# Kernel tuning notes

Measured on AMD Instinct MI355X. Metric: run time of the kernel, lower is better.

The kernel has to match this reference:

```python
import jax, jax.numpy as jnp
import numpy as np

N_NODES = 40000
N_EDGES = 320000
N_GRAPHS = 64
IN_DIM = 128
HID4 = 256   # hidden_dim * 4
OUT_DIM = 128
LN_EPS = 1e-5


def setup_inputs() -> dict:
    key = jax.random.key(0)
    ks = jax.random.split(key, 12)
    x = jax.random.normal(ks[0], (N_NODES, IN_DIM), dtype=jnp.float32)
    w = jax.random.uniform(ks[1], (N_EDGES, 4), dtype=jnp.float32)
    src = jax.random.randint(ks[2], (N_EDGES,), 0, N_NODES, dtype=jnp.int32)
    dst = jax.random.randint(ks[3], (N_EDGES,), 0, N_NODES, dtype=jnp.int32)
    graph_ids = jnp.sort(jax.random.randint(ks[4], (N_NODES,), 0, N_GRAPHS, dtype=jnp.int32))
    # parameters (no biases on GraphConv / fc1 linear)
    W1 = jax.random.normal(ks[5], (IN_DIM, HID4), dtype=jnp.float32) / np.sqrt(IN_DIM)
    fc1_W = jax.random.normal(ks[6], (IN_DIM, HID4), dtype=jnp.float32) / np.sqrt(IN_DIM)
    ln_gamma = jnp.ones((HID4,), dtype=jnp.float32)
    ln_beta = jnp.zeros((HID4,), dtype=jnp.float32)
    W2 = jax.random.normal(ks[7], (2 * HID4, HID4), dtype=jnp.float32) / np.sqrt(2 * HID4)
    W3 = jax.random.normal(ks[8], (HID4, OUT_DIM), dtype=jnp.float32) / np.sqrt(HID4)
    return {"x": x, "w": w, "W1": W1, "fc1_W": fc1_W, "ln_gamma": ln_gamma,
            "ln_beta": ln_beta, "W2": W2, "W3": W3,
            "src": src, "dst": dst, "graph_ids": graph_ids}


def _graph_conv(feat, src, dst, ew, W, out_inv_sqrt, in_inv_sqrt):
    # DGL GraphConv, norm='both', bias=False, with scalar edge_weight:
    # h = D_out^{-1/2} x ; m_e = w_e * h[src] ; agg = scatter_add(m, dst) ;
    # out = (D_in^{-1/2} agg) @ W
    h = feat * out_inv_sqrt[:, None]
    m = h[src] * ew[:, None]                       # [E, D] messages
    agg = jax.ops.segment_sum(m, dst, num_segments=N_NODES)
    return (agg * in_inv_sqrt[:, None]) @ W


def reference(x, w, W1, fc1_W, ln_gamma, ln_beta, W2, W3, src, dst, graph_ids):
    # unweighted degree normalization (DGL uses structural degrees, clamp(min=1))
    ones_e = jnp.ones((N_EDGES,), dtype=x.dtype)
    out_deg = jnp.maximum(jax.ops.segment_sum(ones_e, src, num_segments=N_NODES), 1.0)
    in_deg = jnp.maximum(jax.ops.segment_sum(ones_e, dst, num_segments=N_NODES), 1.0)
    out_inv = out_deg ** -0.5
    in_inv = in_deg ** -0.5

    ew = jnp.max(w, axis=1)                        # [E]

    x1 = jax.nn.relu(_graph_conv(x, src, dst, ew, W1, out_inv, in_inv))

    # fc1: Linear(no bias) -> LayerNorm(affine) -> ReLU
    f1 = x @ fc1_W
    mu = jnp.mean(f1, axis=-1, keepdims=True)
    var = jnp.mean((f1 - mu) ** 2, axis=-1, keepdims=True)
    f1 = (f1 - mu) * jax.lax.rsqrt(var + LN_EPS) * ln_gamma + ln_beta
    f1 = jax.nn.relu(f1)

    x1f1 = jnp.concatenate([x1, f1], axis=1)       # [N, 512]
    x2 = jax.nn.relu(_graph_conv(x1f1, src, dst, ew, W2, out_inv, in_inv))
    x3 = jax.nn.relu(_graph_conv(x2, src, dst, ew, W3, out_inv, in_inv))

    # dgl.sum_nodes over batched graph, then row-wise L2 normalize
    readout = jax.ops.segment_sum(x3, graph_ids, num_segments=N_GRAPHS)  # [G, OUT_DIM]
    norm = jnp.maximum(jnp.linalg.norm(readout, axis=1, keepdims=True), 1e-12)
    return readout / norm
```

## Files before the change

### kernel.cpp

```cpp
#include <hip/hip_runtime.h>

#define N_NODES 40000
#define M_PAD   40064
#define N_EDGES 320000
#define N_GRAPHS 64
#define IN_DIM 128
#define HID4 256
#define OUT_DIM 128
#define LN_EPS 1e-5f

typedef short  s16x8  __attribute__((ext_vector_type(8)));
typedef __bf16 bf16x8 __attribute__((ext_vector_type(8)));
typedef float  f32x4  __attribute__((ext_vector_type(4)));

__device__ __forceinline__ unsigned short f2b(float f) {
    unsigned int u = __builtin_bit_cast(unsigned int, f);
    u += 0x7fffu + ((u >> 16) & 1u);
    return (unsigned short)(u >> 16);
}
__device__ __forceinline__ float b2f(unsigned short h) {
    unsigned int u = (unsigned int)h << 16;
    return __builtin_bit_cast(float, u);
}
__device__ __forceinline__ float lo2f(unsigned int u) { return b2f((unsigned short)u); }
__device__ __forceinline__ float hi2f(unsigned int u) { return b2f((unsigned short)(u >> 16)); }
__device__ __forceinline__ unsigned int packb(float x, float y) {
    return (unsigned int)f2b(x) | ((unsigned int)f2b(y) << 16);
}

__device__ __forceinline__ void gll16(const unsigned short* g, short* lds_base) {
    __builtin_amdgcn_global_load_lds(
        (const __attribute__((address_space(1))) unsigned int*)g,
        (__attribute__((address_space(3))) unsigned int*)lds_base, 16, 0, 0);
}

#define MFMA_BF16(a, b, c) __builtin_amdgcn_mfma_f32_16x16x32_bf16( \
    __builtin_bit_cast(bf16x8, a), __builtin_bit_cast(bf16x8, b), c, 0, 0, 0)


#define XN (N_NODES * IN_DIM)
#define XT (XN / 8)
#define WN 229376
#define PREP_TOT (XT + WN + N_EDGES)

__global__ void prep_all(const float* __restrict__ x, const float* __restrict__ W1,
                         const float* __restrict__ fc1, const float* __restrict__ W2,
                         const float* __restrict__ W3, const float* __restrict__ w,
                         const int* __restrict__ src, const int* __restrict__ dst,
                         unsigned short* __restrict__ xb, unsigned short* __restrict__ W1t,
                         unsigned short* __restrict__ fc1t, unsigned short* __restrict__ W2t,
                         unsigned short* __restrict__ W3t, float* __restrict__ ew,
                         int* __restrict__ cnt_out, int* __restrict__ cnt_in,
                         int* __restrict__ rank) {
    int idx = blockIdx.x * 256 + threadIdx.x;
    if (idx < XT) {
        const float4* xv = (const float4*)x;
        float4 u = xv[idx * 2], v = xv[idx * 2 + 1];
        uint4 o;
        o.x = packb(u.x, u.y); o.y = packb(u.z, u.w);
        o.z = packb(v.x, v.y); o.w = packb(v.z, v.w);
        ((uint4*)xb)[idx] = o;
        return;
    }
    int j = idx - XT;
    if (j < 32768) { int k = j >> 8, n = j & 255; W1t[n * 128 + k] = f2b(W1[j]); return; }
    j -= 32768;
    if (j < 32768) { int k = j >> 8, n = j & 255; fc1t[n * 128 + k] = f2b(fc1[j]); return; }
    j -= 32768;
    if (j < 131072) { int k = j >> 8, n = j & 255; W2t[n * 512 + k] = f2b(W2[j]); return; }
    j -= 131072;
    if (j < 32768) { int k = j >> 7, n = j & 127; W3t[n * 256 + k] = f2b(W3[j]); return; }
    j -= 32768;
    if (j < N_EDGES) {
        float4 v = ((const float4*)w)[j];
        ew[j] = fmaxf(fmaxf(v.x, v.y), fmaxf(v.z, v.w));
        atomicAdd(&cnt_out[src[j]], 1);
        rank[j] = atomicAdd(&cnt_in[dst[j]], 1);
    }
}

__global__ void scan_part(const int* __restrict__ cnt, int* __restrict__ partial) {
    int b = blockIdx.x;
    int s = 0;
    for (int i = threadIdx.x; i < 1000; i += 256) s += cnt[b * 1000 + i];
#pragma unroll
    for (int m = 1; m < 64; m <<= 1) s += __shfl_xor(s, m);
    __shared__ int wsm[4];
    if ((threadIdx.x & 63) == 0) wsm[threadIdx.x >> 6] = s;
    __syncthreads();
    if (threadIdx.x == 0) partial[b] = wsm[0] + wsm[1] + wsm[2] + wsm[3];
}

__global__ void scan_final(const int* __restrict__ cnt_in, const int* __restrict__ cnt_out,
                           const int* __restrict__ partial, int* __restrict__ off,
                           float* __restrict__ out_inv, float* __restrict__ in_inv) {
    int b = blockIdx.x, tid = threadIdx.x;
    int lane = tid & 63, wv = tid >> 6;
    int pre = 0;
    for (int j = 0; j < b; ++j) pre += partial[j];
    int i = b * 1000 + tid;
    int v = (tid < 1000) ? cnt_in[i] : 0;
    int x = v;
#pragma unroll
    for (int ofs = 1; ofs < 64; ofs <<= 1) {
        int t = __shfl_up(x, ofs);
        if (lane >= ofs) x += t;
    }
    __shared__ int wsum[16];
    if (lane == 63) wsum[wv] = x;
    __syncthreads();
    if (wv == 0 && lane < 16) {
        int s = wsum[lane];
#pragma unroll
        for (int ofs = 1; ofs < 16; ofs <<= 1) {
            int t = __shfl_up(s, ofs);
            if (lane >= ofs) s += t;
        }
        wsum[lane] = s;
    }
    __syncthreads();
    int incl = pre + (wv > 0 ? wsum[wv - 1] : 0) + x;
    if (tid < 1000) {
        off[i] = incl - v;
        in_inv[i] = rsqrtf(fmaxf((float)v, 1.0f));
        out_inv[i] = rsqrtf(fmaxf((float)cnt_out[i], 1.0f));
    }
    if (b == 39 && tid == 999) off[N_NODES] = incl;
}

__global__ void csr_fill(const int* __restrict__ src, const int* __restrict__ dst,
                         const float* __restrict__ ew, const float* __restrict__ out_inv,
                         const int* __restrict__ off, const int* __restrict__ rank,
                         int4* __restrict__ es) {
    int e = blockIdx.x * 256 + threadIdx.x;
    if (e >= N_EDGES) return;
    int d = dst[e];
    int slot = off[d] + rank[e];
    int s = src[e];
    float wv = ew[e];
    es[slot] = make_int4(s, __float_as_int(wv * out_inv[s]), __float_as_int(wv), 0);
}


template <int D, int RELU, int WSEL>
__global__ void gather_nodes(const unsigned short* __restrict__ h, const int* __restrict__ off,
                             const int4* __restrict__ eg, const float* __restrict__ scale,
                             unsigned short* __restrict__ outb) {
    int n = blockIdx.x;
    int lane = threadIdx.x;
    int b = off[n], e = off[n + 1];
    const uint2* hu = (const uint2*)h;
    float a0 = 0.f, a1 = 0.f, a2 = 0.f, a3 = 0.f;
    if constexpr (D == 256) {
        int i = b;
        for (; i + 3 < e; i += 4) {
            int4 e0 = eg[i], e1 = eg[i + 1], e2 = eg[i + 2], e3 = eg[i + 3];
            uint2 p0 = hu[(size_t)e0.x * 64 + lane];
            uint2 p1 = hu[(size_t)e1.x * 64 + lane];
            uint2 p2 = hu[(size_t)e2.x * 64 + lane];
            uint2 p3 = hu[(size_t)e3.x * 64 + lane];
            float w0 = __int_as_float(WSEL ? e0.z : e0.y);
            float w1 = __int_as_float(WSEL ? e1.z : e1.y);
            float w2 = __int_as_float(WSEL ? e2.z : e2.y);
            float w3 = __int_as_float(WSEL ? e3.z : e3.y);
            a0 += w0 * lo2f(p0.x) + w1 * lo2f(p1.x) + w2 * lo2f(p2.x) + w3 * lo2f(p3.x);
            a1 += w0 * hi2f(p0.x) + w1 * hi2f(p1.x) + w2 * hi2f(p2.x) + w3 * hi2f(p3.x);
            a2 += w0 * lo2f(p0.y) + w1 * lo2f(p1.y) + w2 * lo2f(p2.y) + w3 * lo2f(p3.y);
            a3 += w0 * hi2f(p0.y) + w1 * hi2f(p1.y) + w2 * hi2f(p2.y) + w3 * hi2f(p3.y);
        }
        for (; i < e; ++i) {
            int4 ee = eg[i];
            uint2 p = hu[(size_t)ee.x * 64 + lane];
            float w0 = __int_as_float(WSEL ? ee.z : ee.y);
            a0 += w0 * lo2f(p.x); a1 += w0 * hi2f(p.x);
            a2 += w0 * lo2f(p.y); a3 += w0 * hi2f(p.y);
        }
        float sc = scale[n];
        a0 *= sc; a1 *= sc; a2 *= sc; a3 *= sc;
        if (RELU) {
            a0 = fmaxf(a0, 0.f); a1 = fmaxf(a1, 0.f);
            a2 = fmaxf(a2, 0.f); a3 = fmaxf(a3, 0.f);
        }
        uint2 o; o.x = packb(a0, a1); o.y = packb(a2, a3);
        ((uint2*)outb)[(size_t)n * 64 + lane] = o;
    } else {
        int half = lane >> 5, cl = lane & 31;
        int i = b;
        for (; i + 3 < e; i += 4) {
            int4 ea = eg[i + half];
            int4 eb = eg[i + 2 + half];
            uint2 pa = hu[(size_t)ea.x * 32 + cl];
            uint2 pb = hu[(size_t)eb.x * 32 + cl];
            float wa = __int_as_float(WSEL ? ea.z : ea.y);
            float wb = __int_as_float(WSEL ? eb.z : eb.y);
            a0 += wa * lo2f(pa.x) + wb * lo2f(pb.x);
            a1 += wa * hi2f(pa.x) + wb * hi2f(pb.x);
            a2 += wa * lo2f(pa.y) + wb * lo2f(pb.y);
            a3 += wa * hi2f(pa.y) + wb * hi2f(pb.y);
        }
        for (; i < e; i += 2) {
            int idx = i + half;
            int4 ee = eg[idx < e ? idx : i];
            float w = (idx < e) ? __int_as_float(WSEL ? ee.z : ee.y) : 0.0f;
            uint2 p = hu[(size_t)ee.x * 32 + cl];
            a0 += w * lo2f(p.x); a1 += w * hi2f(p.x);
            a2 += w * lo2f(p.y); a3 += w * hi2f(p.y);
        }
        a0 += __shfl_xor(a0, 32); a1 += __shfl_xor(a1, 32);
        a2 += __shfl_xor(a2, 32); a3 += __shfl_xor(a3, 32);
        float sc = scale[n];
        a0 *= sc; a1 *= sc; a2 *= sc; a3 *= sc;
        if (RELU) {
            a0 = fmaxf(a0, 0.f); a1 = fmaxf(a1, 0.f);
            a2 = fmaxf(a2, 0.f); a3 = fmaxf(a3, 0.f);
        }
        if (half == 0) {
            uint2 o; o.x = packb(a0, a1); o.y = packb(a2, a3);
            ((uint2*)outb)[(size_t)n * 32 + cl] = o;
        }
    }
}


#define G3_NPB 8

__global__ void gather3_ro(const unsigned short* __restrict__ h, const int* __restrict__ off,
                           const int4* __restrict__ eg, const float* __restrict__ scale,
                           const int* __restrict__ gid, float* __restrict__ ro) {
    int lane = threadIdx.x;
    int half = lane >> 5, cl = lane & 31;
    int n0 = blockIdx.x * G3_NPB;
    int n1 = n0 + G3_NPB;
    if (n1 > N_NODES) n1 = N_NODES;
    const uint2* hu = (const uint2*)h;
    float r0 = 0.f, r1 = 0.f, r2 = 0.f, r3 = 0.f;
    int cur = gid[n0];
    for (int n = n0; n < n1; ++n) {
        int g = gid[n];
        if (g != cur) {
            atomicAdd(&ro[cur * OUT_DIM + 4 * cl + 2 * half], half ? r2 : r0);
            atomicAdd(&ro[cur * OUT_DIM + 4 * cl + 2 * half + 1], half ? r3 : r1);
            r0 = r1 = r2 = r3 = 0.f;
            cur = g;
        }
        int b = off[n], e = off[n + 1];
        float a0 = 0.f, a1 = 0.f, a2 = 0.f, a3 = 0.f;
        int i = b;
        for (; i + 3 < e; i += 4) {
            int4 ea = eg[i + half];
            int4 eb = eg[i + 2 + half];
            uint2 pa = hu[(size_t)ea.x * 32 + cl];
            uint2 pb = hu[(size_t)eb.x * 32 + cl];
            float wa = __int_as_float(ea.z), wb = __int_as_float(eb.z);
            a0 += wa * lo2f(pa.x) + wb * lo2f(pb.x);
            a1 += wa * hi2f(pa.x) + wb * hi2f(pb.x);
            a2 += wa * lo2f(pa.y) + wb * lo2f(pb.y);
            a3 += wa * hi2f(pa.y) + wb * hi2f(pb.y);
        }
        for (; i < e; i += 2) {
            int idx = i + half;
            int4 ee = eg[idx < e ? idx : i];
            float w = (idx < e) ? __int_as_float(ee.z) : 0.0f;
            uint2 p = hu[(size_t)ee.x * 32 + cl];
            a0 += w * lo2f(p.x); a1 += w * hi2f(p.x);
            a2 += w * lo2f(p.y); a3 += w * hi2f(p.y);
        }
        a0 += __shfl_xor(a0, 32); a1 += __shfl_xor(a1, 32);
        a2 += __shfl_xor(a2, 32); a3 += __shfl_xor(a3, 32);
        float sc = scale[n];
        r0 += fmaxf(a0 * sc, 0.0f); r1 += fmaxf(a1 * sc, 0.0f);
        r2 += fmaxf(a2 * sc, 0.0f); r3 += fmaxf(a3 * sc, 0.0f);
    }
    atomicAdd(&ro[cur * OUT_DIM + 4 * cl + 2 * half], half ? r2 : r0);
    atomicAdd(&ro[cur * OUT_DIM + 4 * cl + 2 * half + 1], half ? r3 : r1);
}


__device__ __forceinline__ void gemm_core(short* As, short* Bs,
    const unsigned short* __restrict__ A, const unsigned short* __restrict__ A2,
    const unsigned short* __restrict__ Bt, unsigned short* __restrict__ C,
    const float* __restrict__ rowScaleC, int K1, int K2, int N,
    int relu, int scaleC, int m0, int n0) {
    int tid = threadIdx.x;
    int lane = tid & 63, wave = tid >> 6;
    int wm = (wave >> 1) * 64, wn = (wave & 1) * 64;
    int quad = lane >> 4, r16 = lane & 15;
    const int K = K1 + K2;
    f32x4 acc[4][4] = {};
    int srow = lane >> 3;
    int sk   = ((lane & 7) ^ srow) * 8;
    int xorc = r16 & 7;
    short* ldsA = As + wave * 2048;
    short* ldsB = Bs + wave * 2048;

    for (int k0 = 0; k0 < K; k0 += 64) {
        int kk = k0 + sk;
#pragma unroll
        for (int h = 0; h < 4; ++h) {
            int r = wave * 32 + h * 8 + srow;
            const unsigned short* Ap = (k0 < K1)
                ? A  + (size_t)(m0 + r) * K1 + kk
                : A2 + (size_t)(m0 + r) * K2 + (kk - K1);
            gll16(Ap, ldsA + h * 512);
            gll16(Bt + (size_t)(n0 + r) * K + kk, ldsB + h * 512);
        }
        __syncthreads();
#pragma unroll
        for (int c = 0; c < 2; ++c) {
            s16x8 af[4], bfr[4];
            int pc = (((c * 4 + quad) ^ xorc) << 3);
#pragma unroll
            for (int i = 0; i < 4; ++i)
                af[i] = *(const s16x8*)(As + (wm + i * 16 + r16) * 64 + pc);
#pragma unroll
            for (int j = 0; j < 4; ++j)
                bfr[j] = *(const s16x8*)(Bs + (wn + j * 16 + r16) * 64 + pc);
#pragma unroll
            for (int i = 0; i < 4; ++i)
#pragma unroll
                for (int j = 0; j < 4; ++j)
                    acc[i][j] = MFMA_BF16(af[i], bfr[j], acc[i][j]);
        }
        __syncthreads();
    }

#pragma unroll
    for (int i = 0; i < 4; ++i) {
        int mbase = m0 + wm + i * 16 + quad * 4;
#pragma unroll
        for (int r = 0; r < 4; ++r) {
            int m = mbase + r;
            float sc = scaleC ? rowScaleC[m] : 1.0f;
#pragma unroll
            for (int j = 0; j < 4; ++j) {
                float v = acc[i][j][r] * sc;
                if (relu) v = fmaxf(v, 0.0f);
                C[(size_t)m * N + n0 + wn + j * 16 + r16] = f2b(v);
            }
        }
    }
}

template <int RELU, int SCALE_C>
__global__ __launch_bounds__(256) void gemm_mfma(
    const unsigned short* __restrict__ A, const unsigned short* __restrict__ A2,
    const unsigned short* __restrict__ Bt, unsigned short* __restrict__ C,
    const float* __restrict__ rowScaleC, int K1, int K2, int N) {
    __shared__ short As[8192];
    __shared__ short Bs[8192];
    gemm_core(As, Bs, A, A2, Bt, C, rowScaleC, K1, K2, N, RELU, SCALE_C,
              blockIdx.x * 128, blockIdx.y * 128);
}


__global__ __launch_bounds__(512) void gemm_dual(
    const unsigned short* __restrict__ A0, const unsigned short* __restrict__ B0,
    unsigned short* __restrict__ C0,
    const unsigned short* __restrict__ A1, const unsigned short* __restrict__ B1,
    unsigned short* __restrict__ C1,
    const float* __restrict__ gamma, const float* __restrict__ beta) {
    __shared__ short As[4096];
    __shared__ short Bs[8192];
    __shared__ float lns[128][4];
    __shared__ float lnq[128][4];
    const unsigned short* A  = blockIdx.z ? A1 : A0;
    const unsigned short* Bt = blockIdx.z ? B1 : B0;
    unsigned short* C        = blockIdx.z ? C1 : C0;
    int tid = threadIdx.x;
    int lane = tid & 63, wave = tid >> 6;
    int wm = (wave >> 2) * 64, wn = (wave & 3) * 64;
    int quad = lane >> 4, r16 = lane & 15;
    int m0 = blockIdx.x * 128;
    f32x4 acc[4][4] = {};
    int lrow = lane >> 2;
    int kc = (lane & 3) * 8;
    short* ldsA = As + wave * 512;
    short* ldsB = Bs + wave * 512;

    for (int k0 = 0; k0 < 128; k0 += 32) {
        int kk = k0 + kc;
        int rr = wave * 16 + lrow;
        gll16(A + (size_t)(m0 + rr) * 128 + kk, ldsA);
        gll16(Bt + (size_t)rr * 128 + kk, ldsB);
        gll16(Bt + (size_t)(128 + rr) * 128 + kk, ldsB + 4096);
        __syncthreads();
        s16x8 af[4], bfr[4];
#pragma unroll
        for (int i = 0; i < 4; ++i)
            af[i] = *(const s16x8*)(As + (wm + i * 16 + r16) * 32 + quad * 8);
#pragma unroll
        for (int j = 0; j < 4; ++j)
            bfr[j] = *(const s16x8*)(Bs + (wn + j * 16 + r16) * 32 + quad * 8);
#pragma unroll
        for (int i = 0; i < 4; ++i)
#pragma unroll
            for (int j = 0; j < 4; ++j)
                acc[i][j] = MFMA_BF16(af[i], bfr[j], acc[i][j]);
        __syncthreads();
    }

    if (blockIdx.z == 0) {
#pragma unroll
        for (int i = 0; i < 4; ++i) {
            int mbase = m0 + wm + i * 16 + quad * 4;
#pragma unroll
            for (int r = 0; r < 4; ++r) {
                int m = mbase + r;
#pragma unroll
                for (int j = 0; j < 4; ++j)
                    C[(size_t)m * 256 + wn + j * 16 + r16] = f2b(fmaxf(acc[i][j][r], 0.0f));
            }
        }
    } else {
#pragma unroll
        for (int i = 0; i < 4; ++i)
#pragma unroll
            for (int r = 0; r < 4; ++r) {
                float s = 0.0f, q = 0.0f;
#pragma unroll
                for (int j = 0; j < 4; ++j) { float v = acc[i][j][r]; s += v; q += v * v; }
#pragma unroll
                for (int m = 1; m < 16; m <<= 1) { s += __shfl_xor(s, m); q += __shfl_xor(q, m); }
                if (r16 == 0) {
                    int row = wm + i * 16 + quad * 4 + r;
                    lns[row][wave & 3] = s;
                    lnq[row][wave & 3] = q;
                }
            }
        __syncthreads();
#pragma unroll
        for (int i = 0; i < 4; ++i) {
#pragma unroll
            for (int r = 0; r < 4; ++r) {
                int row = wm + i * 16 + quad * 4 + r;
                float s = lns[row][0] + lns[row][1] + lns[row][2] + lns[row][3];
                float q = lnq[row][0] + lnq[row][1] + lnq[row][2] + lnq[row][3];
                float mu = s * (1.0f / HID4);
                float var = q * (1.0f / HID4) - mu * mu;
                float rs = rsqrtf(var + LN_EPS);
                int m = m0 + row;
#pragma unroll
                for (int j = 0; j < 4; ++j) {
                    int col = wn + j * 16 + r16;
                    float v = (acc[i][j][r] - mu) * rs * gamma[col] + beta[col];
                    C[(size_t)m * 256 + col] = f2b(fmaxf(v, 0.0f));
                }
            }
        }
    }
}


__global__ void normalize_out(const float* __restrict__ ro, float* __restrict__ out) {
    int g = blockIdx.x;
    int d = threadIdx.x;
    float v = ro[g * OUT_DIM + d];
    float ss = v * v;
#pragma unroll
    for (int m = 1; m < 64; m <<= 1) ss += __shfl_xor(ss, m);
    __shared__ float s2[2];
    if ((d & 63) == 0) s2[d >> 6] = ss;
    __syncthreads();
    float tot = s2[0] + s2[1];
    float norm = fmaxf(sqrtf(tot), 1e-12f);
    out[g * OUT_DIM + d] = v / norm;
}


extern "C" void kernel_launch(void* const* d_in, const int* in_sizes, int n_in,
                              void* d_out, int out_size, void* d_ws, size_t ws_size,
                              hipStream_t stream) {
    const float* x    = (const float*)d_in[0];
    const float* w    = (const float*)d_in[1];
    const float* W1   = (const float*)d_in[2];
    const float* fc1W = (const float*)d_in[3];
    const float* gam  = (const float*)d_in[4];
    const float* bet  = (const float*)d_in[5];
    const float* W2   = (const float*)d_in[6];
    const float* W3   = (const float*)d_in[7];
    const int* src = (const int*)d_in[8];
    const int* dst = (const int*)d_in[9];
    const int* gid = (const int*)d_in[10];
    float* out = (float*)d_out;

    float* ws = (float*)d_ws;
    float* out_inv = ws + 0;
    float* in_inv  = ws + 40000;
    float* ew      = ws + 80000;
    int*   cnt_out = (int*)(ws + 400000);
    int*   cnt_in  = (int*)(ws + 440000);
    float* ro      = ws + 480000;
    unsigned short* W1t  = (unsigned short*)(ws + 488192);
    unsigned short* fc1t = (unsigned short*)(ws + 504576);
    unsigned short* W2t  = (unsigned short*)(ws + 520960);
    unsigned short* W3t  = (unsigned short*)(ws + 586496);
    int*   partial = (int*)(ws + 602880);
    int*   off     = (int*)(ws + 602920);
    int4*  es      = (int4*)(ws + 642924);
    unsigned short* xb    = (unsigned short*)(ws + 1923000);
    unsigned short* Q3b   = xb;
    unsigned short* agg1b = (unsigned short*)(ws + 4487100);
    unsigned short* x2b   = agg1b;
    unsigned short* x1b   = (unsigned short*)(ws + 9615300);
    unsigned short* f1b   = (unsigned short*)(ws + 14743500);
    unsigned short* P2b   = (unsigned short*)(ws + 19871700);
    int*   rank    = (int*)(ws + 25000000);

    hipMemsetAsync(cnt_out, 0, (2 * 40000 + N_GRAPHS * OUT_DIM) * sizeof(float), stream);

    prep_all<<<(PREP_TOT + 255) / 256, 256, 0, stream>>>(x, W1, fc1W, W2, W3, w, src, dst,
                                                         xb, W1t, fc1t, W2t, W3t, ew,
                                                         cnt_out, cnt_in, rank);
    scan_part<<<40, 256, 0, stream>>>(cnt_in, partial);
    scan_final<<<40, 1024, 0, stream>>>(cnt_in, cnt_out, partial, off, out_inv, in_inv);
    csr_fill<<<(N_EDGES + 255) / 256, 256, 0, stream>>>(src, dst, ew, out_inv, off, rank, es);

    gather_nodes<IN_DIM, 0, 0><<<N_NODES, 64, 0, stream>>>(xb, off, es, in_inv, agg1b);
    {
        dim3 grid(M_PAD / 128, 1, 2);
        gemm_dual<<<grid, 512, 0, stream>>>(agg1b, W1t, x1b, xb, fc1t, f1b, gam, bet);
    }

    {
        dim3 grid(M_PAD / 128, HID4 / 128);
        gemm_mfma<0, 1><<<grid, 256, 0, stream>>>(x1b, f1b, W2t, P2b, out_inv,
                                                  HID4, HID4, HID4);
    }
    gather_nodes<HID4, 1, 1><<<N_NODES, 64, 0, stream>>>(P2b, off, es, in_inv, x2b);

    {
        dim3 grid(M_PAD / 128, OUT_DIM / 128);
        gemm_mfma<0, 1><<<grid, 256, 0, stream>>>(x2b, nullptr, W3t, Q3b, out_inv,
                                                  HID4, 0, OUT_DIM);
    }
    gather3_ro<<<(N_NODES + G3_NPB - 1) / G3_NPB, 64, 0, stream>>>(Q3b, off, es, in_inv,
                                                                   gid, ro);
    normalize_out<<<N_GRAPHS, 128, 0, stream>>>(ro, out);
}
```

Measured before the change: 273.6 us.

## Co-schedule first-layer gather with fc1 GEMM+LayerNorm in one launch

Merges the layer-1 neighbor gather and the independent fc1 GEMM with LayerNorm into a single kernel. The first 313 blocks run the fc1 tile GEMM and the remaining blocks each gather 8 nodes, one wave per node, with each half-wave handling alternate edges. The conv1 GEMM becomes its own launch after the gather. This lets the memory-bound gather overlap with the MFMA-bound fc1 work and packs several nodes per block instead of one 64-thread block per node, at the cost of a heterogeneous kernel with 512-thread blocks for the gather.

```diff
diff --git a/kernel.cpp b/kernel.cpp
--- a/kernel.cpp
+++ b/kernel.cpp
@@ -139,6 +139,127 @@
     int s = src[e];
     float wv = ew[e];
     es[slot] = make_int4(s, __float_as_int(wv * out_inv[s]), __float_as_int(wv), 0);
+}
+
+
+__global__ __launch_bounds__(512) void g1_fc1(
+    const unsigned short* __restrict__ xb, const int* __restrict__ off,
+    const int4* __restrict__ es, const float* __restrict__ in_inv,
+    unsigned short* __restrict__ agg1b,
+    const unsigned short* __restrict__ fc1t, unsigned short* __restrict__ f1b,
+    const float* __restrict__ gamma, const float* __restrict__ beta) {
+    __shared__ short As[4096];
+    __shared__ short Bs[8192];
+    __shared__ float lns[128][4];
+    __shared__ float lnq[128][4];
+    int tid = threadIdx.x;
+    int lane = tid & 63, wave = tid >> 6;
+
+    if (blockIdx.x >= 313) {
+        int n = (blockIdx.x - 313) * 8 + wave;
+        if (n >= N_NODES) return;
+        int b = off[n], e = off[n + 1];
+        const uint2* hu = (const uint2*)xb;
+        int half = lane >> 5, cl = lane & 31;
+        float a0 = 0.f, a1 = 0.f, a2 = 0.f, a3 = 0.f;
+        int i = b;
+        for (; i + 3 < e; i += 4) {
+            int4 ea = es[i + half];
+            int4 eb = es[i + 2 + half];
+            uint2 pa = hu[(size_t)ea.x * 32 + cl];
+            uint2 pb = hu[(size_t)eb.x * 32 + cl];
+            float wa = __int_as_float(ea.y);
+            float wb = __int_as_float(eb.y);
+            a0 += wa * lo2f(pa.x) + wb * lo2f(pb.x);
+            a1 += wa * hi2f(pa.x) + wb * hi2f(pb.x);
+            a2 += wa * lo2f(pa.y) + wb * lo2f(pb.y);
+            a3 += wa * hi2f(pa.y) + wb * hi2f(pb.y);
+        }
+        for (; i < e; i += 2) {
+            int idx = i + half;
+            int4 ee = es[idx < e ? idx : i];
+            float w = (idx < e) ? __int_as_float(ee.y) : 0.0f;
+            uint2 p = hu[(size_t)ee.x * 32 + cl];
+            a0 += w * lo2f(p.x); a1 += w * hi2f(p.x);
+            a2 += w * lo2f(p.y); a3 += w * hi2f(p.y);
+        }
+        a0 += __shfl_xor(a0, 32); a1 += __shfl_xor(a1, 32);
+        a2 += __shfl_xor(a2, 32); a3 += __shfl_xor(a3, 32);
+        float sc = in_inv[n];
+        a0 *= sc; a1 *= sc; a2 *= sc; a3 *= sc;
+        if (half == 0) {
+            uint2 o; o.x = packb(a0, a1); o.y = packb(a2, a3);
+            ((uint2*)agg1b)[(size_t)n * 32 + cl] = o;
+        }
+        return;
+    }
+
+    int m0 = blockIdx.x * 128;
+    int wm = (wave >> 2) * 64, wn = (wave & 3) * 64;
+    int quad = lane >> 4, r16 = lane & 15;
+    f32x4 acc[4][4] = {};
+    int lrow = lane >> 2;
+    int kc = (lane & 3) * 8;
+    short* ldsA = As + wave * 512;
+    short* ldsB = Bs + wave * 512;
+
+    for (int k0 = 0; k0 < 128; k0 += 32) {
+        int kk = k0 + kc;
+        int rr = wave * 16 + lrow;
+        gll16(xb + (size_t)(m0 + rr) * 128 + kk, ldsA);
+        gll16(fc1t + (size_t)rr * 128 + kk, ldsB);
+        gll16(fc1t + (size_t)(128 + rr) * 128 + kk, ldsB + 4096);
+        __syncthreads();
+        s16x8 af[4], bfr[4];
+#pragma unroll
+        for (int i = 0; i < 4; ++i)
+            af[i] = *(const s16x8*)(As + (wm + i * 16 + r16) * 32 + quad * 8);
+#pragma unroll
+        for (int j = 0; j < 4; ++j)
+            bfr[j] = *(const s16x8*)(Bs + (wn + j * 16 + r16) * 32 + quad * 8);
+#pragma unroll
+        for (int i = 0; i < 4; ++i)
+#pragma unroll
+            for (int j = 0; j < 4; ++j)
+                acc[i][j] = MFMA_BF16(af[i], bfr[j], acc[i][j]);
+        __syncthreads();
+    }
+
+#pragma unroll
+    for (int i = 0; i < 4; ++i)
+#pragma unroll
+        for (int r = 0; r < 4; ++r) {
+            float s = 0.0f, q = 0.0f;
+#pragma unroll
+            for (int j = 0; j < 4; ++j) { float v = acc[i][j][r]; s += v; q += v * v; }
+#pragma unroll
+            for (int m = 1; m < 16; m <<= 1) { s += __shfl_xor(s, m); q += __shfl_xor(q, m); }
+            if (r16 == 0) {
+                int row = wm + i * 16 + quad * 4 + r;
+                lns[row][wave & 3] = s;
+                lnq[row][wave & 3] = q;
+            }
+        }
+    __syncthreads();
+#pragma unroll
+    for (int i = 0; i < 4; ++i) {
+#pragma unroll
+        for (int r = 0; r < 4; ++r) {
+            int row = wm + i * 16 + quad * 4 + r;
+            float s = lns[row][0] + lns[row][1] + lns[row][2] + lns[row][3];
+            float q = lnq[row][0] + lnq[row][1] + lnq[row][2] + lnq[row][3];
+            float mu = s * (1.0f / HID4);
+            float var = q * (1.0f / HID4) - mu * mu;
+            float rs = rsqrtf(var + LN_EPS);
+            int m = m0 + row;
+#pragma unroll
+            for (int j = 0; j < 4; ++j) {
+                int col = wn + j * 16 + r16;
+                float v = (acc[i][j][r] - mu) * rs * gamma[col] + beta[col];
+                f1b[(size_t)m * 256 + col] = f2b(fmaxf(v, 0.0f));
+            }
+        }
+    }
 }
 
 
@@ -353,19 +474,11 @@
 }
 
 
-__global__ __launch_bounds__(512) void gemm_dual(
-    const unsigned short* __restrict__ A0, const unsigned short* __restrict__ B0,
-    unsigned short* __restrict__ C0,
-    const unsigned short* __restrict__ A1, const unsigned short* __restrict__ B1,
-    unsigned short* __restrict__ C1,
-    const float* __restrict__ gamma, const float* __restrict__ beta) {
+__global__ __launch_bounds__(512) void gemm_conv1(
+    const unsigned short* __restrict__ A, const unsigned short* __restrict__ Bt,
+    unsigned short* __restrict__ C) {
     __shared__ short As[4096];
     __shared__ short Bs[8192];
-    __shared__ float lns[128][4];
-    __shared__ float lnq[128][4];
-    const unsigned short* A  = blockIdx.z ? A1 : A0;
-    const unsigned short* Bt = blockIdx.z ? B1 : B0;
-    unsigned short* C        = blockIdx.z ? C1 : C0;
     int tid = threadIdx.x;
     int lane = tid & 63, wave = tid >> 6;
     int wm = (wave >> 2) * 64, wn = (wave & 3) * 64;
@@ -399,53 +512,15 @@
         __syncthreads();
     }
 
-    if (blockIdx.z == 0) {
-#pragma unroll
-        for (int i = 0; i < 4; ++i) {
-            int mbase = m0 + wm + i * 16 + quad * 4;
-#pragma unroll
-            for (int r = 0; r < 4; ++r) {
-                int m = mbase + r;
-#pragma unroll
-                for (int j = 0; j < 4; ++j)
-                    C[(size_t)m * 256 + wn + j * 16 + r16] = f2b(fmaxf(acc[i][j][r], 0.0f));
-            }
-        }
-    } else {
-#pragma unroll
-        for (int i = 0; i < 4; ++i)
-#pragma unroll
-            for (int r = 0; r < 4; ++r) {
-                float s = 0.0f, q = 0.0f;
-#pragma unroll
-                for (int j = 0; j < 4; ++j) { float v = acc[i][j][r]; s += v; q += v * v; }
-#pragma unroll
-                for (int m = 1; m < 16; m <<= 1) { s += __shfl_xor(s, m); q += __shfl_xor(q, m); }
-                if (r16 == 0) {
-                    int row = wm + i * 16 + quad * 4 + r;
-                    lns[row][wave & 3] = s;
-                    lnq[row][wave & 3] = q;
-                }
-            }
-        __syncthreads();
-#pragma unroll
-        for (int i = 0; i < 4; ++i) {
-#pragma unroll
-            for (int r = 0; r < 4; ++r) {
-                int row = wm + i * 16 + quad * 4 + r;
-                float s = lns[row][0] + lns[row][1] + lns[row][2] + lns[row][3];
-                float q = lnq[row][0] + lnq[row][1] + lnq[row][2] + lnq[row][3];
-                float mu = s * (1.0f / HID4);
-                float var = q * (1.0f / HID4) - mu * mu;
-                float rs = rsqrtf(var + LN_EPS);
-                int m = m0 + row;
-#pragma unroll
-                for (int j = 0; j < 4; ++j) {
-                    int col = wn + j * 16 + r16;
-                    float v = (acc[i][j][r] - mu) * rs * gamma[col] + beta[col];
-                    C[(size_t)m * 256 + col] = f2b(fmaxf(v, 0.0f));
-                }
-            }
+#pragma unroll
+    for (int i = 0; i < 4; ++i) {
+        int mbase = m0 + wm + i * 16 + quad * 4;
+#pragma unroll
+        for (int r = 0; r < 4; ++r) {
+            int m = mbase + r;
+#pragma unroll
+            for (int j = 0; j < 4; ++j)
+                C[(size_t)m * 256 + wn + j * 16 + r16] = f2b(fmaxf(acc[i][j][r], 0.0f));
         }
     }
 }
@@ -515,11 +590,9 @@
     scan_final<<<40, 1024, 0, stream>>>(cnt_in, cnt_out, partial, off, out_inv, in_inv);
     csr_fill<<<(N_EDGES + 255) / 256, 256, 0, stream>>>(src, dst, ew, out_inv, off, rank, es);
 
-    gather_nodes<IN_DIM, 0, 0><<<N_NODES, 64, 0, stream>>>(xb, off, es, in_inv, agg1b);
-    {
-        dim3 grid(M_PAD / 128, 1, 2);
-        gemm_dual<<<grid, 512, 0, stream>>>(agg1b, W1t, x1b, xb, fc1t, f1b, gam, bet);
-    }
+    g1_fc1<<<313 + 5000, 512, 0, stream>>>(xb, off, es, in_inv, agg1b,
+                                           fc1t, f1b, gam, bet);
+    gemm_conv1<<<313, 512, 0, stream>>>(agg1b, W1t, x1b);
 
     {
         dim3 grid(M_PAD / 128, HID4 / 128);
```

Measured after the change: 312.6 us. 14.3% more time.
